# Kernel optimization log

Measured on AMD Instinct MI355X. Metric: run time of the kernel, lower is better.

The kernel has to match this reference:

```python
import jax, jax.numpy as jnp
import numpy as np

DIM = 256
HEADS = 8
WINDOWS = (1, 2, 4)
B, H, W = 1, 64, 64


def _integral(a):
    # double cumsum over last two dims, then zero-pad one row/col at top/left
    s = jnp.cumsum(jnp.cumsum(a, axis=-2), axis=-1)
    pad = [(0, 0)] * (a.ndim - 2) + [(1, 0), (1, 0)]
    return jnp.pad(s, pad)


def _box(P, ws, Ho, Wo):
    # replicate-pad then box-difference; equivalent to the 2x2 [[1,-1],[-1,1]]
    # kernel conv2d with dilation=ws applied in the torch module.
    tp = ws - 1
    r = tp // 2
    l = tp - r
    pad = [(0, 0)] * (P.ndim - 2) + [(l, r), (l, r)]
    Pp = jnp.pad(P, pad, mode='edge')
    return (Pp[..., ws:ws + Ho, ws:ws + Wo] - Pp[..., ws:ws + Ho, :Wo]
            - Pp[..., :Ho, ws:ws + Wo] + Pp[..., :Ho, :Wo])


def setup_inputs() -> dict:
    key = jax.random.key(0)
    ks = jax.random.split(key, 6)
    x = jax.random.normal(ks[0], (B, DIM, H, W), jnp.float32)
    Wq = jax.random.normal(ks[1], (DIM, DIM), jnp.float32) * 0.05
    Wk = jax.random.normal(ks[2], (DIM, DIM), jnp.float32) * 0.05
    Wv = jax.random.normal(ks[3], (DIM, DIM), jnp.float32) * 0.05
    Wout = jax.random.normal(ks[4], (DIM, DIM * len(WINDOWS)), jnp.float32) * 0.05
    bout = jnp.zeros((DIM,), jnp.float32)
    return {"x": x, "Wq": Wq, "Wk": Wk, "Wv": Wv, "Wout": Wout, "bout": bout}


def reference(x, Wq, Wk, Wv, Wout, bout):
    b, C, Hh, Ww = x.shape
    h = HEADS
    d = C // h
    # 1x1 convs (no bias)
    q = jnp.einsum('bchw,oc->bohw', x, Wq).reshape(b * h, d, Hh, Ww)
    k = jnp.einsum('bchw,oc->bohw', x, Wk).reshape(b * h, d, Hh, Ww)
    v = jnp.einsum('bchw,oc->bohw', x, Wv).reshape(b * h, d, Hh, Ww)
    q = jax.nn.sigmoid(q)
    k = jax.nn.sigmoid(k)
    v = v / jnp.maximum(jnp.linalg.norm(v, axis=1, keepdims=True), 1e-12)

    Ik = _integral(k)                                  # (bh, d, H+1, W+1)
    Ikv = _integral(jnp.einsum('bfhw,bghw->bfghw', k, v))  # (bh, d, d, H+1, W+1)

    outs = []
    for w in WINDOWS:
        ws = Hh // w
        wk = _box(Ik, ws, Hh, Ww)    # (bh, d, H, W)
        wkv = _box(Ikv, ws, Hh, Ww)  # (bh, d, d, H, W)
        attn = jnp.einsum('bdhw,bdfhw->bfhw', q, wkv)
        norm = jnp.einsum('bdhw,bdhw->bhw', q, wk)
        attn = attn / (norm[:, None] + 1e-6)
        outs.append(attn.reshape(b, C, Hh, Ww))
    o = jnp.concatenate(outs, axis=1)  # (b, C*len(WINDOWS), H, W)
    return jnp.einsum('bchw,oc->bohw', o, Wout) + bout[None, :, None, None]
```

## Files before the change

### kernel.cpp

```cpp
#include <hip/hip_runtime.h>
#include <math.h>

#define NPIX 4096
#define CHSZ 3145728
#define NRMSZ 98304

template <int CTRL, int RM>
__device__ __forceinline__ float dpp_add(float x) {
    int xi = __builtin_bit_cast(int, x);
    int sh = __builtin_amdgcn_update_dpp(0, xi, CTRL, RM, 0xf, false);
    return x + __builtin_bit_cast(float, sh);
}

__device__ __forceinline__ float wave_iscan(float x) {
    x = dpp_add<0x111, 0xf>(x);
    x = dpp_add<0x112, 0xf>(x);
    x = dpp_add<0x114, 0xf>(x);
    x = dpp_add<0x118, 0xf>(x);
    x = dpp_add<0x142, 0xa>(x);
    x = dpp_add<0x143, 0xc>(x);
    return x;
}

__device__ __forceinline__ void lds_barrier() {
    asm volatile("s_waitcnt lgkmcnt(0)" ::: "memory");
    __builtin_amdgcn_s_barrier();
    __builtin_amdgcn_sched_barrier(0);
}

__global__ __launch_bounds__(256) void qkv_kernel(
    const float* __restrict__ x, const float* __restrict__ Wq,
    const float* __restrict__ Wk, const float* __restrict__ Wv,
    float* __restrict__ qo, float* __restrict__ ko, float* __restrict__ vo)
{
    const int pt = blockIdx.x * 128;
    const int ot = blockIdx.y * 32;
    const int mat = blockIdx.z;
    const float* __restrict__ W = (mat == 0) ? Wq : ((mat == 1) ? Wk : Wv);
    float* __restrict__ out = (mat == 0) ? qo : ((mat == 1) ? ko : vo);

    __shared__ __align__(16) float Xs[32][132];
    __shared__ __align__(16) float Wt[32][36];

    const int t = threadIdx.x;
    const int pc = t & 31;
    const int oc = t >> 5;
    const int xc = t >> 5;
    const int xp = (t & 31) << 2;
    const int lo = t >> 3;
    const int lg = (t & 7) << 2;

    float4 xf[4];
    float4 wf;
#pragma unroll
    for (int i = 0; i < 4; i++)
        xf[i] = *reinterpret_cast<const float4*>(x + (xc + 8 * i) * NPIX + pt + xp);
    wf = *reinterpret_cast<const float4*>(W + (ot + lo) * 256 + lg);

    float acc[4][4];
#pragma unroll
    for (int j = 0; j < 4; j++)
#pragma unroll
        for (int i = 0; i < 4; i++) acc[j][i] = 0.f;

    for (int kt = 0; kt < 256; kt += 32) {
#pragma unroll
        for (int i = 0; i < 4; i++)
            *reinterpret_cast<float4*>(&Xs[xc + 8 * i][xp]) = xf[i];
        Wt[lg + 0][lo] = wf.x;
        Wt[lg + 1][lo] = wf.y;
        Wt[lg + 2][lo] = wf.z;
        Wt[lg + 3][lo] = wf.w;
        __syncthreads();
        if (kt + 32 < 256) {
#pragma unroll
            for (int i = 0; i < 4; i++)
                xf[i] = *reinterpret_cast<const float4*>(
                    x + (kt + 32 + xc + 8 * i) * NPIX + pt + xp);
            wf = *reinterpret_cast<const float4*>(W + (ot + lo) * 256 + kt + 32 + lg);
        }
#pragma unroll
        for (int kk = 0; kk < 32; kk++) {
            float4 a = *reinterpret_cast<const float4*>(&Xs[kk][pc << 2]);
            float av[4] = {a.x, a.y, a.z, a.w};
            float4 b4 = *reinterpret_cast<const float4*>(&Wt[kk][oc << 2]);
            float bv[4] = {b4.x, b4.y, b4.z, b4.w};
#pragma unroll
            for (int j = 0; j < 4; j++)
#pragma unroll
                for (int i = 0; i < 4; i++)
                    acc[j][i] = fmaf(bv[j], av[i], acc[j][i]);
        }
        __syncthreads();
    }

    if (mat < 2) {
#pragma unroll
        for (int j = 0; j < 4; j++) {
            const int o = ot + (oc << 2) + j;
            float4 r;
            r.x = 1.f / (1.f + __expf(-acc[j][0]));
            r.y = 1.f / (1.f + __expf(-acc[j][1]));
            r.z = 1.f / (1.f + __expf(-acc[j][2]));
            r.w = 1.f / (1.f + __expf(-acc[j][3]));
            *reinterpret_cast<float4*>(out + o * NPIX + pt + (pc << 2)) = r;
        }
    } else {
        float* scratch = &Xs[0][0];
#pragma unroll
        for (int i = 0; i < 4; i++) {
            float ss = 0.f;
#pragma unroll
            for (int j = 0; j < 4; j++) ss += acc[j][i] * acc[j][i];
            scratch[oc * 128 + (pc << 2) + i] = ss;
        }
        __syncthreads();
        float scale[4];
#pragma unroll
        for (int i = 0; i < 4; i++) {
            float tot = 0.f;
#pragma unroll
            for (int g = 0; g < 8; g++) tot += scratch[g * 128 + (pc << 2) + i];
            scale[i] = 1.f / fmaxf(sqrtf(tot), 1e-12f);
        }
#pragma unroll
        for (int j = 0; j < 4; j++) {
            const int o = ot + (oc << 2) + j;
            float4 r;
            r.x = acc[j][0] * scale[0];
            r.y = acc[j][1] * scale[1];
            r.z = acc[j][2] * scale[2];
            r.w = acc[j][3] * scale[3];
            *reinterpret_cast<float4*>(out + o * NPIX + pt + (pc << 2)) = r;
        }
    }
}

template <int PD>
__global__ __launch_bounds__(512) void attn_kernel(
    const float* __restrict__ q, const float* __restrict__ k,
    const float* __restrict__ v, float* __restrict__ num, float* __restrict__ nrm)
{
    const int f = blockIdx.x;
    const int head = blockIdx.y;
    const int dg = blockIdx.z;
    const bool isnorm = (f == 32);

    const float* __restrict__ kh = k + (head * 32 + dg * PD) * NPIX;
    const float* __restrict__ qh = q + (head * 32 + dg * PD) * NPIX;
    const float* __restrict__ vf = v + (head * 32 + (isnorm ? 0 : f)) * NPIX;

    __shared__ __align__(16) float Pt[65][132];
    __shared__ float csum[8][68];

    const int t = threadIdx.x;
    const int lane = t & 63;
    const int wv = t >> 6;

    for (int i = t; i < 65 * 132; i += 512) (&Pt[0][0])[i] = 0.f;

    float vreg[8], kcur[8];
#pragma unroll
    for (int i = 0; i < 8; i++) {
        const int r = wv * 8 + i;
        vreg[i] = isnorm ? 1.f : vf[r * 64 + lane];
        kcur[i] = kh[r * 64 + lane];
    }

    float acc[3][8];
#pragma unroll
    for (int w = 0; w < 3; w++)
#pragma unroll
        for (int i = 0; i < 8; i++) acc[w][i] = 0.f;

    lds_barrier();

    for (int dd = 0; dd < PD; dd++) {
        float qv[8];
#pragma unroll
        for (int g = 0; g < 2; g++)
#pragma unroll
            for (int j = 0; j < 4; j++)
                qv[g * 4 + j] = qh[dd * NPIX + ((wv + 8 * g) * 4 + j) * 64 + lane];

        float pv[8];
        float run = 0.f;
#pragma unroll
        for (int i = 0; i < 8; i++) {
            float rs = wave_iscan(kcur[i] * vreg[i]);
            pv[i] = run;
            run += rs;
        }
        if (dd + 1 < PD) {
#pragma unroll
            for (int i = 0; i < 8; i++)
                kcur[i] = kh[(dd + 1) * NPIX + (wv * 8 + i) * 64 + lane];
        }
        csum[wv][lane] = run;
        lds_barrier();
        float off = 0.f;
#pragma unroll
        for (int w2 = 0; w2 < 7; w2++) if (w2 < wv) off += csum[w2][lane];
#pragma unroll
        for (int i = 0; i < 8; i++) pv[i] += off;
#pragma unroll
        for (int s = 0; s < 2; s++) {
            float4 r4 = make_float4(pv[4 * s], pv[4 * s + 1], pv[4 * s + 2], pv[4 * s + 3]);
            *reinterpret_cast<float4*>(&Pt[lane + 1][32 + wv * 8 + 4 * s]) = r4;
        }
        if (wv == 7) {
            const float tot = off + run;
            const float4 p4 = make_float4(tot, tot, tot, tot);
#pragma unroll
            for (int s = 0; s < 8; s++)
                *reinterpret_cast<float4*>(&Pt[lane + 1][96 + 4 * s]) = p4;
        }
        lds_barrier();
#pragma unroll
        for (int g = 0; g < 2; g++) {
            const int y0 = (wv + 8 * g) * 4;
#pragma unroll
            for (int w = 0; w < 3; w++) {
                const int hw = 32 >> w;
                const int xlo = max(lane - hw, 0);
                const int xhi = min(lane + hw, 64);
                const int ylo = 32 + y0 - hw;
                const int yhi = 32 + y0 + hw;
                float4 A4 = *reinterpret_cast<const float4*>(&Pt[xhi][yhi]);
                float4 B4 = *reinterpret_cast<const float4*>(&Pt[xlo][yhi]);
                float4 C4, E4;
                if (y0 + 3 <= hw) {
                    C4 = make_float4(0.f, 0.f, 0.f, 0.f);
                    E4 = C4;
                } else {
                    C4 = *reinterpret_cast<const float4*>(&Pt[xhi][ylo]);
                    E4 = *reinterpret_cast<const float4*>(&Pt[xlo][ylo]);
                }
                acc[w][g * 4 + 0] = fmaf(qv[g * 4 + 0], (A4.x - B4.x) - (C4.x - E4.x), acc[w][g * 4 + 0]);
                acc[w][g * 4 + 1] = fmaf(qv[g * 4 + 1], (A4.y - B4.y) - (C4.y - E4.y), acc[w][g * 4 + 1]);
                acc[w][g * 4 + 2] = fmaf(qv[g * 4 + 2], (A4.z - B4.z) - (C4.z - E4.z), acc[w][g * 4 + 2]);
                acc[w][g * 4 + 3] = fmaf(qv[g * 4 + 3], (A4.w - B4.w) - (C4.w - E4.w), acc[w][g * 4 + 3]);
            }
        }
    }

    float* __restrict__ nout = num + (size_t)dg * CHSZ;
    float* __restrict__ rout = nrm + (size_t)dg * NRMSZ;
#pragma unroll
    for (int w = 0; w < 3; w++) {
#pragma unroll
        for (int g = 0; g < 2; g++) {
#pragma unroll
            for (int j = 0; j < 4; j++) {
                const int px = ((wv + 8 * g) * 4 + j) * 64 + lane;
                const float val = acc[w][g * 4 + j];
                if (isnorm) rout[(w * 8 + head) * NPIX + px] = val;
                else        nout[((w * 8 + head) * 32 + f) * NPIX + px] = val;
            }
        }
    }
}

template <int NS>
__global__ __launch_bounds__(256) void out_kernel(
    const float* __restrict__ num, const float* __restrict__ nrm,
    const float* __restrict__ Wout, const float* __restrict__ bout,
    float* __restrict__ out)
{
    const int pt = blockIdx.x * 64;
    const int ot = blockIdx.y * 32;
    __shared__ __align__(16) float As[32][68];
    __shared__ __align__(16) float Wt[32][36];
    const int t = threadIdx.x;
    const int pc = t & 15;
    const int oc = t >> 4;
    const int xc = t >> 4;
    const int xp = (t & 15) << 2;
    const int lo = t >> 3;
    const int lg = (t & 7) << 2;

    float4 nv[NS][2], mv[NS], wf;
#pragma unroll
    for (int s = 0; s < NS; s++) {
#pragma unroll
        for (int i = 0; i < 2; i++)
            nv[s][i] = *reinterpret_cast<const float4*>(
                num + (size_t)s * CHSZ + (size_t)(xc + 16 * i) * NPIX + pt + xp);
        mv[s] = *reinterpret_cast<const float4*>(nrm + (size_t)s * NRMSZ + pt + xp);
    }
    wf = *reinterpret_cast<const float4*>(Wout + (ot + lo) * 768 + lg);

    float acc[2][4];
#pragma unroll
    for (int j = 0; j < 2; j++)
#pragma unroll
        for (int i = 0; i < 4; i++) acc[j][i] = 0.f;

    for (int kt = 0; kt < 24; kt++) {
        float4 ms = mv[0];
#pragma unroll
        for (int s = 1; s < NS; s++) {
            ms.x += mv[s].x; ms.y += mv[s].y; ms.z += mv[s].z; ms.w += mv[s].w;
        }
        float4 rv;
        rv.x = 1.f / (ms.x + 1e-6f); rv.y = 1.f / (ms.y + 1e-6f);
        rv.z = 1.f / (ms.z + 1e-6f); rv.w = 1.f / (ms.w + 1e-6f);
#pragma unroll
        for (int i = 0; i < 2; i++) {
            float4 r = nv[0][i];
#pragma unroll
            for (int s = 1; s < NS; s++) {
                r.x += nv[s][i].x; r.y += nv[s][i].y;
                r.z += nv[s][i].z; r.w += nv[s][i].w;
            }
            r.x *= rv.x; r.y *= rv.y; r.z *= rv.z; r.w *= rv.w;
            *reinterpret_cast<float4*>(&As[xc + 16 * i][xp]) = r;
        }
        Wt[lg + 0][lo] = wf.x;
        Wt[lg + 1][lo] = wf.y;
        Wt[lg + 2][lo] = wf.z;
        Wt[lg + 3][lo] = wf.w;
        __syncthreads();
        if (kt + 1 < 24) {
#pragma unroll
            for (int s = 0; s < NS; s++) {
#pragma unroll
                for (int i = 0; i < 2; i++)
                    nv[s][i] = *reinterpret_cast<const float4*>(
                        num + (size_t)s * CHSZ +
                        (size_t)((kt + 1) * 32 + xc + 16 * i) * NPIX + pt + xp);
                mv[s] = *reinterpret_cast<const float4*>(
                    nrm + (size_t)s * NRMSZ + (kt + 1) * NPIX + pt + xp);
            }
            wf = *reinterpret_cast<const float4*>(Wout + (ot + lo) * 768 + (kt + 1) * 32 + lg);
        }
#pragma unroll
        for (int kk = 0; kk < 32; kk++) {
            float4 a = *reinterpret_cast<const float4*>(&As[kk][pc << 2]);
            float2 b2 = *reinterpret_cast<const float2*>(&Wt[kk][oc << 1]);
            acc[0][0] = fmaf(b2.x, a.x, acc[0][0]);
            acc[0][1] = fmaf(b2.x, a.y, acc[0][1]);
            acc[0][2] = fmaf(b2.x, a.z, acc[0][2]);
            acc[0][3] = fmaf(b2.x, a.w, acc[0][3]);
            acc[1][0] = fmaf(b2.y, a.x, acc[1][0]);
            acc[1][1] = fmaf(b2.y, a.y, acc[1][1]);
            acc[1][2] = fmaf(b2.y, a.z, acc[1][2]);
            acc[1][3] = fmaf(b2.y, a.w, acc[1][3]);
        }
        __syncthreads();
    }

#pragma unroll
    for (int j = 0; j < 2; j++) {
        const int o = ot + (oc << 1) + j;
        const float bb = bout[o];
        float4 r;
        r.x = acc[j][0] + bb;
        r.y = acc[j][1] + bb;
        r.z = acc[j][2] + bb;
        r.w = acc[j][3] + bb;
        *reinterpret_cast<float4*>(out + o * NPIX + pt + (pc << 2)) = r;
    }
}

extern "C" void kernel_launch(void* const* d_in, const int* in_sizes, int n_in,
                              void* d_out, int out_size, void* d_ws, size_t ws_size,
                              hipStream_t stream)
{
    const float* x    = (const float*)d_in[0];
    const float* Wq   = (const float*)d_in[1];
    const float* Wk   = (const float*)d_in[2];
    const float* Wv   = (const float*)d_in[3];
    const float* Wout = (const float*)d_in[4];
    const float* bout = (const float*)d_in[5];
    float* out = (float*)d_out;

    float* ws = (float*)d_ws;
    float* q   = ws;
    float* k   = ws + 1048576;
    float* v   = ws + 2097152;
    float* num = ws + 3145728;
    const size_t fl = ws_size / 4;

    qkv_kernel<<<dim3(32, 8, 3), 256, 0, stream>>>(x, Wq, Wk, Wv, q, k, v);

    if (fl >= 3145728 + (size_t)4 * (CHSZ + NRMSZ)) {
        float* nrm = num + (size_t)4 * CHSZ;
        attn_kernel<8><<<dim3(33, 8, 4), 512, 0, stream>>>(q, k, v, num, nrm);
        out_kernel<4><<<dim3(64, 8), 256, 0, stream>>>(num, nrm, Wout, bout, out);
    } else if (fl >= 3145728 + (size_t)2 * (CHSZ + NRMSZ)) {
        float* nrm = num + (size_t)2 * CHSZ;
        attn_kernel<16><<<dim3(33, 8, 2), 512, 0, stream>>>(q, k, v, num, nrm);
        out_kernel<2><<<dim3(64, 8), 256, 0, stream>>>(num, nrm, Wout, bout, out);
    } else {
        float* nrm = num + CHSZ;
        attn_kernel<32><<<dim3(33, 8, 1), 512, 0, stream>>>(q, k, v, num, nrm);
        out_kernel<1><<<dim3(64, 8), 256, 0, stream>>>(num, nrm, Wout, bout, out);
    }
}
```

Before: 149.0 us.

## Widen out_kernel tile to 64 outputs and drop the four-way attention split

```diff
diff --git a/kernel.cpp b/kernel.cpp
--- a/kernel.cpp
+++ b/kernel.cpp
@@ -107,6 +107,7 @@
         }
     } else {
         float* scratch = &Xs[0][0];
+        __syncthreads();
 #pragma unroll
         for (int i = 0; i < 4; i++) {
             float ss = 0.f;
@@ -262,33 +263,31 @@
 }
 
 template <int NS>
-__global__ __launch_bounds__(256) void out_kernel(
+__global__ __launch_bounds__(512) void out_kernel(
     const float* __restrict__ num, const float* __restrict__ nrm,
     const float* __restrict__ Wout, const float* __restrict__ bout,
     float* __restrict__ out)
 {
     const int pt = blockIdx.x * 64;
-    const int ot = blockIdx.y * 32;
+    const int ot = blockIdx.y * 64;
     __shared__ __align__(16) float As[32][68];
-    __shared__ __align__(16) float Wt[32][36];
+    __shared__ __align__(16) float Wt[32][68];
     const int t = threadIdx.x;
     const int pc = t & 15;
     const int oc = t >> 4;
     const int xc = t >> 4;
     const int xp = (t & 15) << 2;
-    const int lo = t >> 3;
-    const int lg = (t & 7) << 2;
-
-    float4 nv[NS][2], mv[NS], wf;
+    const int lo = t & 63;
+    const int lc = (t >> 6) << 2;
+
+    float4 nv[NS], mv[NS], wf;
 #pragma unroll
     for (int s = 0; s < NS; s++) {
-#pragma unroll
-        for (int i = 0; i < 2; i++)
-            nv[s][i] = *reinterpret_cast<const float4*>(
-                num + (size_t)s * CHSZ + (size_t)(xc + 16 * i) * NPIX + pt + xp);
+        nv[s] = *reinterpret_cast<const float4*>(
+            num + (size_t)s * CHSZ + (size_t)xc * NPIX + pt + xp);
         mv[s] = *reinterpret_cast<const float4*>(nrm + (size_t)s * NRMSZ + pt + xp);
     }
-    wf = *reinterpret_cast<const float4*>(Wout + (ot + lo) * 768 + lg);
+    wf = *reinterpret_cast<const float4*>(Wout + (ot + lo) * 768 + lc);
 
     float acc[2][4];
 #pragma unroll
@@ -302,37 +301,30 @@
         for (int s = 1; s < NS; s++) {
             ms.x += mv[s].x; ms.y += mv[s].y; ms.z += mv[s].z; ms.w += mv[s].w;
         }
-        float4 rv;
-        rv.x = 1.f / (ms.x + 1e-6f); rv.y = 1.f / (ms.y + 1e-6f);
-        rv.z = 1.f / (ms.z + 1e-6f); rv.w = 1.f / (ms.w + 1e-6f);
-#pragma unroll
-        for (int i = 0; i < 2; i++) {
-            float4 r = nv[0][i];
-#pragma unroll
-            for (int s = 1; s < NS; s++) {
-                r.x += nv[s][i].x; r.y += nv[s][i].y;
-                r.z += nv[s][i].z; r.w += nv[s][i].w;
-            }
-            r.x *= rv.x; r.y *= rv.y; r.z *= rv.z; r.w *= rv.w;
-            *reinterpret_cast<float4*>(&As[xc + 16 * i][xp]) = r;
-        }
-        Wt[lg + 0][lo] = wf.x;
-        Wt[lg + 1][lo] = wf.y;
-        Wt[lg + 2][lo] = wf.z;
-        Wt[lg + 3][lo] = wf.w;
+        float4 r = nv[0];
+#pragma unroll
+        for (int s = 1; s < NS; s++) {
+            r.x += nv[s].x; r.y += nv[s].y; r.z += nv[s].z; r.w += nv[s].w;
+        }
+        r.x /= (ms.x + 1e-6f); r.y /= (ms.y + 1e-6f);
+        r.z /= (ms.z + 1e-6f); r.w /= (ms.w + 1e-6f);
+        *reinterpret_cast<float4*>(&As[xc][xp]) = r;
+        Wt[lc + 0][lo] = wf.x;
+        Wt[lc + 1][lo] = wf.y;
+        Wt[lc + 2][lo] = wf.z;
+        Wt[lc + 3][lo] = wf.w;
         __syncthreads();
         if (kt + 1 < 24) {
 #pragma unroll
             for (int s = 0; s < NS; s++) {
-#pragma unroll
-                for (int i = 0; i < 2; i++)
-                    nv[s][i] = *reinterpret_cast<const float4*>(
-                        num + (size_t)s * CHSZ +
-                        (size_t)((kt + 1) * 32 + xc + 16 * i) * NPIX + pt + xp);
+                nv[s] = *reinterpret_cast<const float4*>(
+                    num + (size_t)s * CHSZ +
+                    (size_t)((kt + 1) * 32 + xc) * NPIX + pt + xp);
                 mv[s] = *reinterpret_cast<const float4*>(
                     nrm + (size_t)s * NRMSZ + (kt + 1) * NPIX + pt + xp);
             }
-            wf = *reinterpret_cast<const float4*>(Wout + (ot + lo) * 768 + (kt + 1) * 32 + lg);
+            wf = *reinterpret_cast<const float4*>(
+                Wout + (ot + lo) * 768 + (kt + 1) * 32 + lc);
         }
 #pragma unroll
         for (int kk = 0; kk < 32; kk++) {
@@ -384,17 +376,13 @@
 
     qkv_kernel<<<dim3(32, 8, 3), 256, 0, stream>>>(x, Wq, Wk, Wv, q, k, v);
 
-    if (fl >= 3145728 + (size_t)4 * (CHSZ + NRMSZ)) {
-        float* nrm = num + (size_t)4 * CHSZ;
-        attn_kernel<8><<<dim3(33, 8, 4), 512, 0, stream>>>(q, k, v, num, nrm);
-        out_kernel<4><<<dim3(64, 8), 256, 0, stream>>>(num, nrm, Wout, bout, out);
-    } else if (fl >= 3145728 + (size_t)2 * (CHSZ + NRMSZ)) {
+    if (fl >= 3145728 + (size_t)2 * (CHSZ + NRMSZ)) {
         float* nrm = num + (size_t)2 * CHSZ;
         attn_kernel<16><<<dim3(33, 8, 2), 512, 0, stream>>>(q, k, v, num, nrm);
-        out_kernel<2><<<dim3(64, 8), 256, 0, stream>>>(num, nrm, Wout, bout, out);
+        out_kernel<2><<<dim3(64, 4), 512, 0, stream>>>(num, nrm, Wout, bout, out);
     } else {
         float* nrm = num + CHSZ;
         attn_kernel<32><<<dim3(33, 8, 1), 512, 0, stream>>>(q, k, v, num, nrm);
-        out_kernel<1><<<dim3(64, 8), 256, 0, stream>>>(num, nrm, Wout, bout, out);
-    }
-}
+        out_kernel<1><<<dim3(64, 4), 512, 0, stream>>>(num, nrm, Wout, bout, out);
+    }
+}
```

Result: slower. 153.5 us (+3.0%).

## Widen output-projection tile and split K across two partial buffers with merge

Applied to the files above, without the earlier changes.

```diff
diff --git a/kernel.cpp b/kernel.cpp
--- a/kernel.cpp
+++ b/kernel.cpp
@@ -107,6 +107,7 @@
         }
     } else {
         float* scratch = &Xs[0][0];
+        __syncthreads();
 #pragma unroll
         for (int i = 0; i < 4; i++) {
             float ss = 0.f;
@@ -264,39 +265,41 @@
 template <int NS>
 __global__ __launch_bounds__(256) void out_kernel(
     const float* __restrict__ num, const float* __restrict__ nrm,
-    const float* __restrict__ Wout, const float* __restrict__ bout,
-    float* __restrict__ out)
+    const float* __restrict__ Wout, float* __restrict__ obuf)
 {
     const int pt = blockIdx.x * 64;
-    const int ot = blockIdx.y * 32;
+    const int ot = blockIdx.y * 64;
+    const int kt0 = blockIdx.z * 12;
     __shared__ __align__(16) float As[32][68];
-    __shared__ __align__(16) float Wt[32][36];
+    __shared__ __align__(16) float Wt[32][68];
     const int t = threadIdx.x;
     const int pc = t & 15;
     const int oc = t >> 4;
     const int xc = t >> 4;
     const int xp = (t & 15) << 2;
-    const int lo = t >> 3;
-    const int lg = (t & 7) << 2;
-
-    float4 nv[NS][2], mv[NS], wf;
+    const int lo = t & 63;
+    const int lc = (t >> 6) << 2;
+
+    float4 nv[NS][2], mv[NS], wf[2];
 #pragma unroll
     for (int s = 0; s < NS; s++) {
 #pragma unroll
         for (int i = 0; i < 2; i++)
             nv[s][i] = *reinterpret_cast<const float4*>(
-                num + (size_t)s * CHSZ + (size_t)(xc + 16 * i) * NPIX + pt + xp);
-        mv[s] = *reinterpret_cast<const float4*>(nrm + (size_t)s * NRMSZ + pt + xp);
-    }
-    wf = *reinterpret_cast<const float4*>(Wout + (ot + lo) * 768 + lg);
-
-    float acc[2][4];
-#pragma unroll
-    for (int j = 0; j < 2; j++)
+                num + (size_t)s * CHSZ + (size_t)(kt0 * 32 + xc + 16 * i) * NPIX + pt + xp);
+        mv[s] = *reinterpret_cast<const float4*>(
+            nrm + (size_t)s * NRMSZ + kt0 * NPIX + pt + xp);
+    }
+    wf[0] = *reinterpret_cast<const float4*>(Wout + (ot + lo) * 768 + kt0 * 32 + lc);
+    wf[1] = *reinterpret_cast<const float4*>(Wout + (ot + lo) * 768 + kt0 * 32 + lc + 16);
+
+    float acc[4][4];
+#pragma unroll
+    for (int j = 0; j < 4; j++)
 #pragma unroll
         for (int i = 0; i < 4; i++) acc[j][i] = 0.f;
 
-    for (int kt = 0; kt < 24; kt++) {
+    for (int kt = kt0; kt < kt0 + 12; kt++) {
         float4 ms = mv[0];
 #pragma unroll
         for (int s = 1; s < NS; s++) {
@@ -316,12 +319,15 @@
             r.x *= rv.x; r.y *= rv.y; r.z *= rv.z; r.w *= rv.w;
             *reinterpret_cast<float4*>(&As[xc + 16 * i][xp]) = r;
         }
-        Wt[lg + 0][lo] = wf.x;
-        Wt[lg + 1][lo] = wf.y;
-        Wt[lg + 2][lo] = wf.z;
-        Wt[lg + 3][lo] = wf.w;
-        __syncthreads();
-        if (kt + 1 < 24) {
+#pragma unroll
+        for (int i = 0; i < 2; i++) {
+            Wt[lc + 16 * i + 0][lo] = wf[i].x;
+            Wt[lc + 16 * i + 1][lo] = wf[i].y;
+            Wt[lc + 16 * i + 2][lo] = wf[i].z;
+            Wt[lc + 16 * i + 3][lo] = wf[i].w;
+        }
+        __syncthreads();
+        if (kt + 1 < kt0 + 12) {
 #pragma unroll
             for (int s = 0; s < NS; s++) {
 #pragma unroll
@@ -332,35 +338,50 @@
                 mv[s] = *reinterpret_cast<const float4*>(
                     nrm + (size_t)s * NRMSZ + (kt + 1) * NPIX + pt + xp);
             }
-            wf = *reinterpret_cast<const float4*>(Wout + (ot + lo) * 768 + (kt + 1) * 32 + lg);
+            wf[0] = *reinterpret_cast<const float4*>(
+                Wout + (ot + lo) * 768 + (kt + 1) * 32 + lc);
+            wf[1] = *reinterpret_cast<const float4*>(
+                Wout + (ot + lo) * 768 + (kt + 1) * 32 + lc + 16);
         }
 #pragma unroll
         for (int kk = 0; kk < 32; kk++) {
             float4 a = *reinterpret_cast<const float4*>(&As[kk][pc << 2]);
-            float2 b2 = *reinterpret_cast<const float2*>(&Wt[kk][oc << 1]);
-            acc[0][0] = fmaf(b2.x, a.x, acc[0][0]);
-            acc[0][1] = fmaf(b2.x, a.y, acc[0][1]);
-            acc[0][2] = fmaf(b2.x, a.z, acc[0][2]);
-            acc[0][3] = fmaf(b2.x, a.w, acc[0][3]);
-            acc[1][0] = fmaf(b2.y, a.x, acc[1][0]);
-            acc[1][1] = fmaf(b2.y, a.y, acc[1][1]);
-            acc[1][2] = fmaf(b2.y, a.z, acc[1][2]);
-            acc[1][3] = fmaf(b2.y, a.w, acc[1][3]);
-        }
-        __syncthreads();
-    }
-
-#pragma unroll
-    for (int j = 0; j < 2; j++) {
-        const int o = ot + (oc << 1) + j;
-        const float bb = bout[o];
+            float av[4] = {a.x, a.y, a.z, a.w};
+            float4 b4 = *reinterpret_cast<const float4*>(&Wt[kk][oc << 2]);
+            float bv[4] = {b4.x, b4.y, b4.z, b4.w};
+#pragma unroll
+            for (int j = 0; j < 4; j++)
+#pragma unroll
+                for (int i = 0; i < 4; i++)
+                    acc[j][i] = fmaf(bv[j], av[i], acc[j][i]);
+        }
+        __syncthreads();
+    }
+
+    float* __restrict__ ob = obuf + (size_t)blockIdx.z * 1048576;
+#pragma unroll
+    for (int j = 0; j < 4; j++) {
+        const int o = ot + (oc << 2) + j;
         float4 r;
-        r.x = acc[j][0] + bb;
-        r.y = acc[j][1] + bb;
-        r.z = acc[j][2] + bb;
-        r.w = acc[j][3] + bb;
-        *reinterpret_cast<float4*>(out + o * NPIX + pt + (pc << 2)) = r;
-    }
+        r.x = acc[j][0]; r.y = acc[j][1]; r.z = acc[j][2]; r.w = acc[j][3];
+        *reinterpret_cast<float4*>(ob + o * NPIX + pt + (pc << 2)) = r;
+    }
+}
+
+__global__ __launch_bounds__(256) void kmerge_kernel(
+    const float* __restrict__ obuf, const float* __restrict__ bout,
+    float* __restrict__ out)
+{
+    const int i4 = (blockIdx.x * 256 + threadIdx.x) * 4;
+    const float bb = bout[i4 >> 12];
+    float4 a = *reinterpret_cast<const float4*>(obuf + i4);
+    float4 b = *reinterpret_cast<const float4*>(obuf + 1048576 + i4);
+    float4 r;
+    r.x = a.x + b.x + bb;
+    r.y = a.y + b.y + bb;
+    r.z = a.z + b.z + bb;
+    r.w = a.w + b.w + bb;
+    *reinterpret_cast<float4*>(out + i4) = r;
 }
 
 extern "C" void kernel_launch(void* const* d_in, const int* in_sizes, int n_in,
@@ -380,6 +401,7 @@
     float* k   = ws + 1048576;
     float* v   = ws + 2097152;
     float* num = ws + 3145728;
+    float* obuf = ws;
     const size_t fl = ws_size / 4;
 
     qkv_kernel<<<dim3(32, 8, 3), 256, 0, stream>>>(x, Wq, Wk, Wv, q, k, v);
@@ -387,14 +409,15 @@
     if (fl >= 3145728 + (size_t)4 * (CHSZ + NRMSZ)) {
         float* nrm = num + (size_t)4 * CHSZ;
         attn_kernel<8><<<dim3(33, 8, 4), 512, 0, stream>>>(q, k, v, num, nrm);
-        out_kernel<4><<<dim3(64, 8), 256, 0, stream>>>(num, nrm, Wout, bout, out);
+        out_kernel<4><<<dim3(64, 4, 2), 256, 0, stream>>>(num, nrm, Wout, obuf);
     } else if (fl >= 3145728 + (size_t)2 * (CHSZ + NRMSZ)) {
         float* nrm = num + (size_t)2 * CHSZ;
         attn_kernel<16><<<dim3(33, 8, 2), 512, 0, stream>>>(q, k, v, num, nrm);
-        out_kernel<2><<<dim3(64, 8), 256, 0, stream>>>(num, nrm, Wout, bout, out);
+        out_kernel<2><<<dim3(64, 4, 2), 256, 0, stream>>>(num, nrm, Wout, obuf);
     } else {
         float* nrm = num + CHSZ;
         attn_kernel<32><<<dim3(33, 8, 1), 512, 0, stream>>>(q, k, v, num, nrm);
-        out_kernel<1><<<dim3(64, 8), 256, 0, stream>>>(num, nrm, Wout, bout, out);
-    }
-}
+        out_kernel<1><<<dim3(64, 4, 2), 256, 0, stream>>>(num, nrm, Wout, obuf);
+    }
+    kmerge_kernel<<<dim3(1024), 256, 0, stream>>>(obuf, bout, out);
+}
```

Result: faster. 141.7 us, median of 2 (-4.9%).
